# Optimization experiments

Hardware: AMD Instinct MI355X
Metric: run time of the kernel (lower is better)

Reference implementation:

```python
import jax, jax.numpy as jnp
import numpy as np

HIDDEN = 768
PDIM = int(HIDDEN / 4.67)  # 164
QK_DIM = 16
EPS = 1e-5


def setup_inputs() -> dict:
    key = jax.random.key(0)
    k_hs, k_qkv, k_out = jax.random.split(key, 3)
    B, S = 8, 2048
    hidden_states = jax.random.normal(k_hs, (B, S, HIDDEN), dtype=jnp.float32)
    qkv_out = 2 * QK_DIM + PDIM  # 196
    qkv_w = jax.random.normal(k_qkv, (qkv_out, PDIM), dtype=jnp.float32) * (PDIM ** -0.5)
    qkv_b = jnp.zeros((qkv_out,), dtype=jnp.float32)
    out_w = jax.random.normal(k_out, (HIDDEN, HIDDEN), dtype=jnp.float32) * (HIDDEN ** -0.5)
    out_b = jnp.zeros((HIDDEN,), dtype=jnp.float32)
    ln_scale = jnp.ones((PDIM,), dtype=jnp.float32)
    ln_bias = jnp.zeros((PDIM,), dtype=jnp.float32)
    return {
        "hidden_states": hidden_states,
        "ln_scale": ln_scale,
        "ln_bias": ln_bias,
        "qkv_w": qkv_w,
        "qkv_b": qkv_b,
        "out_w": out_w,
        "out_b": out_b,
    }


def reference(hidden_states, ln_scale, ln_bias, qkv_w, qkv_b, out_w, out_b):
    # channel split
    x1 = hidden_states[..., :PDIM]   # [B,S,pdim]
    x2 = hidden_states[..., PDIM:]   # [B,S,hidden-pdim]
    # LayerNorm over last dim
    mean = jnp.mean(x1, axis=-1, keepdims=True)
    var = jnp.mean(jnp.square(x1 - mean), axis=-1, keepdims=True)
    x1n = (x1 - mean) * jax.lax.rsqrt(var + EPS) * ln_scale + ln_bias
    # qkv projection: [B,S,2*qk+pdim]
    qkv = jnp.einsum("bsd,od->bso", x1n, qkv_w) + qkv_b
    q = qkv[..., :QK_DIM]
    k = qkv[..., QK_DIM:2 * QK_DIM]
    v = qkv[..., 2 * QK_DIM:]
    scale = QK_DIM ** -0.5
    scores = jnp.einsum("bqd,bkd->bqk", q, k) * scale  # [B,S,S]
    probs = jax.nn.softmax(scores, axis=-1)
    attended = jnp.einsum("bqk,bkd->bqd", probs, v)  # [B,S,pdim]
    merged = jnp.concatenate([attended, x2], axis=-1)  # [B,S,hidden]
    out = jnp.einsum("bsd,od->bso", merged, out_w) + out_b
    return out
```

## Files before the change

kernel.cpp:

```cpp
#include <hip/hip_runtime.h>
#include <hip/hip_bf16.h>

#define HID 768
#define PD 164
#define NQ 196
#define SEQ 2048

typedef __attribute__((ext_vector_type(8))) short bf16x8_t;
typedef __attribute__((ext_vector_type(4))) float f32x4_t;
typedef __attribute__((ext_vector_type(16))) float f32x16_t;
typedef __attribute__((ext_vector_type(4))) unsigned int u32x4_t;

static __device__ __forceinline__ unsigned short f2bfu(float f) {
  union { __hip_bfloat16 h; unsigned short u; } cv;
  cv.h = __float2bfloat16(f);
  return cv.u;
}

static __device__ __forceinline__ unsigned cvtpk(float a, float b) {
  unsigned r;
  asm("v_cvt_pk_bf16_f32 %0, %1, %2" : "=v"(r) : "v"(a), "v"(b));
  return r;
}

static __device__ __forceinline__ void gload16(const void* g, void* l) {
  __builtin_amdgcn_global_load_lds(
      (const __attribute__((address_space(1))) void*)g,
      (__attribute__((address_space(3))) void*)l, 16, 0, 0);
}

__global__ __launch_bounds__(256) void k_prep(const float* __restrict__ qkv_w,
                                              const float* __restrict__ out_w,
                                              unsigned short* __restrict__ qwb,
                                              unsigned short* __restrict__ wb) {
  int bid = blockIdx.x;
  if (bid < 576) {
    int i = (bid * 256 + threadIdx.x) * 4;
    float4 v = *(const float4*)(out_w + i);
    ushort4 o;
    o.x = f2bfu(v.x); o.y = f2bfu(v.y); o.z = f2bfu(v.z); o.w = f2bfu(v.w);
    *(ushort4*)(wb + i) = o;
  } else {
    int i = ((bid - 576) * 256 + threadIdx.x) * 4;
    int n = i / 192, k = i - n * 192;
    float v0 = (n < NQ && k + 0 < PD) ? qkv_w[n * PD + k + 0] : 0.f;
    float v1 = (n < NQ && k + 1 < PD) ? qkv_w[n * PD + k + 1] : 0.f;
    float v2 = (n < NQ && k + 2 < PD) ? qkv_w[n * PD + k + 2] : 0.f;
    float v3 = (n < NQ && k + 3 < PD) ? qkv_w[n * PD + k + 3] : 0.f;
    ushort4 o;
    o.x = f2bfu(v0); o.y = f2bfu(v1); o.z = f2bfu(v2); o.w = f2bfu(v3);
    *(ushort4*)(qwb + i) = o;
  }
}

__global__ __launch_bounds__(256) void k_ln(const float* __restrict__ hidden,
                                            const float* __restrict__ lns,
                                            const float* __restrict__ lnb,
                                            unsigned short* __restrict__ x1n,
                                            unsigned short* __restrict__ merged) {
  __shared__ float xr[64][172];
  __shared__ float stats[64][2];
  int t = threadIdx.x;
  int r0 = blockIdx.x * 64;
  #pragma unroll
  for (int i = 0; i < 11; i++) {
    int idx = t + i * 256;
    if (idx < 2624) {
      int row = idx / 41, q = idx - row * 41;
      float4 v = *(const float4*)(hidden + (size_t)(r0 + row) * HID + q * 4);
      *(float4*)&xr[row][q * 4] = v;
    }
  }
  __syncthreads();
  {
    int l = t & 63, w = t >> 6;
    int row = w * 16 + (l & 15), g = l >> 4;
    float sum = 0.f, sq = 0.f;
    #pragma unroll
    for (int j = 0; j < 41; j++) {
      float x = xr[row][g * 41 + j];
      sum += x; sq += x * x;
    }
    sum += __shfl_xor(sum, 16, 64); sum += __shfl_xor(sum, 32, 64);
    sq  += __shfl_xor(sq, 16, 64);  sq  += __shfl_xor(sq, 32, 64);
    float mean = sum * (1.f / PD);
    float var = sq * (1.f / PD) - mean * mean;
    float rstd = rsqrtf(var + 1e-5f);
    if (g == 0) { stats[row][0] = mean; stats[row][1] = rstd; }
  }
  __syncthreads();
  #pragma unroll
  for (int i = 0; i < 24; i++) {
    int idx = t + i * 256;
    int row = idx / 96, c2 = idx - row * 96;
    int d = c2 * 2;
    float mean = stats[row][0], rstd = stats[row][1];
    float v0 = (d < PD)     ? (xr[row][d]     - mean) * rstd * lns[d]     + lnb[d]     : 0.f;
    float v1 = (d + 1 < PD) ? (xr[row][d + 1] - mean) * rstd * lns[d + 1] + lnb[d + 1] : 0.f;
    unsigned int pk = (unsigned int)f2bfu(v0) | ((unsigned int)f2bfu(v1) << 16);
    *(unsigned int*)(x1n + (size_t)(r0 + row) * 192 + d) = pk;
  }
  #pragma unroll
  for (int i = 0; i < 38; i++) {
    int idx = t + i * 256;
    if (idx < 9664) {
      int row = idx / 151, q = idx - row * 151;
      int d = PD + q * 4;
      float4 v = *(const float4*)(hidden + (size_t)(r0 + row) * HID + d);
      ushort4 o;
      o.x = f2bfu(v.x); o.y = f2bfu(v.y); o.z = f2bfu(v.z); o.w = f2bfu(v.w);
      *(ushort4*)(merged + (size_t)(r0 + row) * HID + d) = o;
    }
  }
}

__global__ __launch_bounds__(256) void k_qkv(const unsigned short* __restrict__ x1n,
                                             const unsigned short* __restrict__ qwb,
                                             const float* __restrict__ qkv_b,
                                             unsigned short* __restrict__ qg,
                                             unsigned short* __restrict__ kg,
                                             unsigned short* __restrict__ v16) {
  __shared__ unsigned short Al[64 * 64];
  __shared__ unsigned short Bl[208 * 64];
  int t = threadIdx.x;
  int m0 = blockIdx.x * 64;
  int l = t & 63, w = t >> 6;
  f32x4_t acc[13];
  #pragma unroll
  for (int n = 0; n < 13; n++) acc[n] = (f32x4_t){0.f, 0.f, 0.f, 0.f};
  for (int ks = 0; ks < 3; ks++) {
    #pragma unroll
    for (int i = 0; i < 2; i++) {
      int off = t + i * 256;
      int row = off >> 3, c = off & 7;
      gload16(x1n + (size_t)(m0 + row) * 192 + ks * 64 + c * 8, (char*)Al + off * 16);
    }
    #pragma unroll
    for (int i = 0; i < 7; i++) {
      int off = t + i * 256;
      if (off < 1664) {
        int row = off >> 3, c = off & 7;
        gload16(qwb + (size_t)row * 192 + ks * 64 + c * 8, (char*)Bl + off * 16);
      }
    }
    __syncthreads();
    #pragma unroll
    for (int kc = 0; kc < 2; kc++) {
      bf16x8_t a = *(const bf16x8_t*)(Al + (w * 16 + (l & 15)) * 64 + kc * 32 + (l >> 4) * 8);
      #pragma unroll
      for (int n = 0; n < 13; n++) {
        bf16x8_t b = *(const bf16x8_t*)(Bl + (n * 16 + (l & 15)) * 64 + kc * 32 + (l >> 4) * 8);
        acc[n] = __builtin_amdgcn_mfma_f32_16x16x32_bf16(a, b, acc[n], 0, 0, 0);
      }
    }
    __syncthreads();
  }
  int g = l >> 4, lr15 = l & 15;
  {
    float bias = qkv_b[lr15];
    #pragma unroll
    for (int r = 0; r < 4; r++) {
      int grow = m0 + w * 16 + g * 4 + r;
      qg[(size_t)grow * 16 + lr15] = f2bfu((acc[0][r] + bias) * 0.36067376022224085f);
    }
  }
  {
    float bias = qkv_b[16 + lr15];
    #pragma unroll
    for (int r = 0; r < 4; r++) {
      int grow = m0 + w * 16 + g * 4 + r;
      kg[(size_t)grow * 16 + lr15] = f2bfu(acc[1][r] + bias);
    }
  }
  int s0 = (m0 & 2047) + w * 16;
  int bb = m0 >> 11;
  size_t vrowbase = (size_t)(bb * 128 + (s0 >> 4)) * 192;
  #pragma unroll
  for (int n = 2; n < 13; n++) {
    int col = n * 16 + lr15;
    int d = col - 32;
    float bias = (col < NQ) ? qkv_b[col] : 0.f;
    float v0 = acc[n][0] + bias, v1 = acc[n][1] + bias;
    float v2 = acc[n][2] + bias, v3 = acc[n][3] + bias;
    if (d == 164) { v0 = v1 = v2 = v3 = 1.f; }
    else if (d >= PD) { v0 = v1 = v2 = v3 = 0.f; }
    ushort4 o;
    o.x = f2bfu(v0); o.y = f2bfu(v1); o.z = f2bfu(v2); o.w = f2bfu(v3);
    *(ushort4*)(v16 + (vrowbase + d) * 16 + g * 4) = o;
  }
}

__global__ __launch_bounds__(256, 2) void k_attn(const unsigned short* __restrict__ qg,
                                                 const unsigned short* __restrict__ kg,
                                                 const unsigned short* __restrict__ v16,
                                                 unsigned short* __restrict__ merged) {
  __shared__ float red[2][64 * 98];
  int t = threadIdx.x;
  int w = t >> 6, l = t & 63;
  int b = blockIdx.x & 7, qt = blockIdx.x >> 3;
  int lo = l & 31, hi = l >> 5;
  int qbase = b * SEQ + qt * 32;
  bf16x8_t qf = *(const bf16x8_t*)(qg + (size_t)(qbase + lo) * 16 + hi * 8);
  const unsigned short* kb = kg + (size_t)b * SEQ * 16;
  const unsigned short* vbb = v16 + (size_t)b * 128 * 192 * 16;
  f32x16_t zro;
  #pragma unroll
  for (int r = 0; r < 16; r++) zro[r] = 0.f;
  f32x16_t acc[6];
  #pragma unroll
  for (int f = 0; f < 6; f++) acc[f] = zro;

  int it0 = w * 8;
  bf16x8_t kf0 = *(const bf16x8_t*)(kb + (size_t)(it0 * 64 + lo) * 16 + hi * 8);
  bf16x8_t kf1 = *(const bf16x8_t*)(kb + (size_t)(it0 * 64 + 32 + lo) * 16 + hi * 8);
  bf16x8_t va[6], vb_[6];
  {
    const unsigned short* vt0 = vbb + (size_t)(it0 * 4) * (192 * 16) + hi * 8;
    #pragma unroll
    for (int f = 0; f < 6; f++) va[f] = *(const bf16x8_t*)(vt0 + (f * 32 + lo) * 16);
  }
  for (int it = it0; it < it0 + 8; ++it) {
    bf16x8_t nk0 = *(const bf16x8_t*)(kb + (size_t)((it + 1) * 64 + lo) * 16 + hi * 8);
    bf16x8_t nk1 = *(const bf16x8_t*)(kb + (size_t)((it + 1) * 64 + 32 + lo) * 16 + hi * 8);
    f32x16_t sc0 = __builtin_amdgcn_mfma_f32_32x32x16_bf16(kf0, qf, zro, 0, 0, 0);
    f32x16_t sc1 = __builtin_amdgcn_mfma_f32_32x32x16_bf16(kf1, qf, zro, 0, 0, 0);
    bf16x8_t pa[4];
    #pragma unroll
    for (int jt = 0; jt < 2; ++jt) {
      f32x16_t sc = jt ? sc1 : sc0;
      unsigned u[8];
      #pragma unroll
      for (int k = 0; k < 8; ++k)
        u[k] = cvtpk(exp2f(sc[2 * k]), exp2f(sc[2 * k + 1]));
      asm volatile("v_permlane32_swap_b32 %0, %1" : "+v"(u[0]), "+v"(u[2]));
      asm volatile("v_permlane32_swap_b32 %0, %1" : "+v"(u[1]), "+v"(u[3]));
      asm volatile("v_permlane32_swap_b32 %0, %1" : "+v"(u[4]), "+v"(u[6]));
      asm volatile("v_permlane32_swap_b32 %0, %1" : "+v"(u[5]), "+v"(u[7]));
      union { u32x4_t u4; bf16x8_t h8; } c0, c1;
      c0.u4 = (u32x4_t){u[0], u[1], u[2], u[3]};
      c1.u4 = (u32x4_t){u[4], u[5], u[6], u[7]};
      pa[jt * 2 + 0] = c0.h8;
      pa[jt * 2 + 1] = c1.h8;
    }
#define PV_STEP(JS, VCUR, VNXT, NT, NJS)                                            \
    {                                                                               \
      const unsigned short* vtn = vbb + (size_t)((NT) * 4 + (NJS)) * (192 * 16) + hi * 8; \
      _Pragma("unroll")                                                             \
      for (int f = 0; f < 6; f++) VNXT[f] = *(const bf16x8_t*)(vtn + (f * 32 + lo) * 16); \
      _Pragma("unroll")                                                             \
      for (int f = 0; f < 6; f++)                                                   \
        acc[f] = __builtin_amdgcn_mfma_f32_32x32x16_bf16(pa[JS], VCUR[f], acc[f], 0, 0, 0); \
    }
    PV_STEP(0, va,  vb_, it, 1)
    PV_STEP(1, vb_, va,  it, 2)
    PV_STEP(2, va,  vb_, it, 3)
    PV_STEP(3, vb_, va,  it + 1, 0)
#undef PV_STEP
    kf0 = nk0; kf1 = nk1;
  }

  if (w >= 2) {
    float* dst = &red[w - 2][l * 98];
    #pragma unroll
    for (int f = 0; f < 6; f++)
      #pragma unroll
      for (int r = 0; r < 16; r += 2)
        *(float2*)(dst + f * 16 + r) = make_float2(acc[f][r], acc[f][r + 1]);
  }
  __syncthreads();
  if (w < 2) {
    const float* src = &red[w][l * 98];
    #pragma unroll
    for (int f = 0; f < 6; f++)
      #pragma unroll
      for (int r = 0; r < 16; r += 2) {
        float2 v = *(const float2*)(src + f * 16 + r);
        acc[f][r] += v.x; acc[f][r + 1] += v.y;
      }
  }
  __syncthreads();
  if (w == 1) {
    float* dst = &red[0][l * 98];
    #pragma unroll
    for (int f = 0; f < 6; f++)
      #pragma unroll
      for (int r = 0; r < 16; r += 2)
        *(float2*)(dst + f * 16 + r) = make_float2(acc[f][r], acc[f][r + 1]);
  }
  __syncthreads();
  if (w == 0) {
    const float* src = &red[0][l * 98];
    #pragma unroll
    for (int f = 0; f < 6; f++)
      #pragma unroll
      for (int r = 0; r < 16; r += 2) {
        float2 v = *(const float2*)(src + f * 16 + r);
        acc[f][r] += v.x; acc[f][r + 1] += v.y;
      }
    float dninv[16];
    #pragma unroll
    for (int r = 0; r < 16; ++r)
      dninv[r] = 1.0f / __shfl(acc[5][r], 4 + hi * 32, 64);
    #pragma unroll
    for (int f = 0; f < 6; ++f) {
      int d = f * 32 + lo;
      if (d < PD) {
        #pragma unroll
        for (int r = 0; r < 16; ++r) {
          int q = qbase + (r & 3) + 8 * (r >> 2) + 4 * hi;
          merged[(size_t)q * HID + d] = f2bfu(acc[f][r] * dninv[r]);
        }
      }
    }
  }
}

__global__ __launch_bounds__(256) void k_out(const unsigned short* __restrict__ mg,
                                             const unsigned short* __restrict__ wb,
                                             const float* __restrict__ out_b,
                                             float* __restrict__ out) {
  __shared__ unsigned short Al[2][128 * 64];
  __shared__ unsigned short Bl[2][128 * 64];
  int t = threadIdx.x;
  int bid = blockIdx.x;
  int wgid = (bid & 7) * 96 + (bid >> 3);
  int nb = wgid % 6, mb = wgid / 6;
  int m0 = mb * 128, n0 = nb * 128;
  int l = t & 63, w = t >> 6, wr = w >> 1, wc = w & 1;
  int lr = l & 15, lg = l >> 4;
  f32x4_t acc[4][4];
  #pragma unroll
  for (int mi = 0; mi < 4; mi++)
    #pragma unroll
    for (int ni = 0; ni < 4; ni++) acc[mi][ni] = (f32x4_t){0.f, 0.f, 0.f, 0.f};

  auto stage = [&](int buf, int kt) {
    #pragma unroll
    for (int i = 0; i < 4; i++) {
      int off = t + i * 256;
      int row = off >> 3, c = off & 7;
      int cs = c ^ (row & 7);
      gload16(mg + (size_t)(m0 + row) * HID + kt * 64 + cs * 8, (char*)&Al[buf][0] + off * 16);
    }
    #pragma unroll
    for (int i = 0; i < 4; i++) {
      int off = t + i * 256;
      int row = off >> 3, c = off & 7;
      int cs = c ^ (row & 7);
      gload16(wb + (size_t)(n0 + row) * HID + kt * 64 + cs * 8, (char*)&Bl[buf][0] + off * 16);
    }
  };
  auto compute = [&](int cur) {
    __builtin_amdgcn_s_setprio(1);
    #pragma unroll
    for (int kc = 0; kc < 2; kc++) {
      bf16x8_t a[4], bfr[4];
      #pragma unroll
      for (int mi = 0; mi < 4; mi++)
        a[mi] = *(const bf16x8_t*)(&Al[cur][(wr * 64 + mi * 16 + lr) * 64 + (((kc * 4 + lg) ^ (lr & 7)) * 8)]);
      #pragma unroll
      for (int ni = 0; ni < 4; ni++)
        bfr[ni] = *(const bf16x8_t*)(&Bl[cur][(wc * 64 + ni * 16 + lr) * 64 + (((kc * 4 + lg) ^ (lr & 7)) * 8)]);
      #pragma unroll
      for (int mi = 0; mi < 4; mi++)
        #pragma unroll
        for (int ni = 0; ni < 4; ni++)
          acc[mi][ni] = __builtin_amdgcn_mfma_f32_16x16x32_bf16(a[mi], bfr[ni], acc[mi][ni], 0, 0, 0);
    }
    __builtin_amdgcn_s_setprio(0);
  };

  stage(0, 0);
  stage(1, 1);
  for (int kt = 0; kt < 11; kt++) {
    int cur = kt & 1;
    asm volatile("s_waitcnt vmcnt(8)" ::: "memory");
    __builtin_amdgcn_sched_barrier(0);
    __builtin_amdgcn_s_barrier();
    compute(cur);
    asm volatile("s_waitcnt lgkmcnt(0)" ::: "memory");
    __builtin_amdgcn_sched_barrier(0);
    __builtin_amdgcn_s_barrier();
    if (kt + 2 < 12) stage(cur, kt + 2);
  }
  asm volatile("s_waitcnt vmcnt(0)" ::: "memory");
  __builtin_amdgcn_sched_barrier(0);
  __builtin_amdgcn_s_barrier();
  compute(1);

  #pragma unroll
  for (int ni = 0; ni < 4; ni++) {
    int col = n0 + wc * 64 + ni * 16 + lr;
    float bias = out_b[col];
    #pragma unroll
    for (int mi = 0; mi < 4; mi++) {
      #pragma unroll
      for (int r = 0; r < 4; r++) {
        int row = m0 + wr * 64 + mi * 16 + lg * 4 + r;
        out[(size_t)row * HID + col] = acc[mi][ni][r] + bias;
      }
    }
  }
}

extern "C" void kernel_launch(void* const* d_in, const int* in_sizes, int n_in,
                              void* d_out, int out_size, void* d_ws, size_t ws_size,
                              hipStream_t stream) {
  const float* hidden = (const float*)d_in[0];
  const float* lns    = (const float*)d_in[1];
  const float* lnb    = (const float*)d_in[2];
  const float* qkv_w  = (const float*)d_in[3];
  const float* qkv_b  = (const float*)d_in[4];
  const float* out_w  = (const float*)d_in[5];
  const float* out_b  = (const float*)d_in[6];
  char* ws = (char*)d_ws;
  unsigned short* qg  = (unsigned short*)(ws + 0);
  unsigned short* kg  = (unsigned short*)(ws + 524288);
  unsigned short* v16 = (unsigned short*)(ws + 1048576);
  unsigned short* x1n = (unsigned short*)(ws + 7340032);
  unsigned short* qwb = (unsigned short*)(ws + 13631488);
  unsigned short* wb  = (unsigned short*)(ws + 13711360);
  unsigned short* mg  = (unsigned short*)(ws + 14891008);
  hipLaunchKernelGGL(k_prep, dim3(615), dim3(256), 0, stream, qkv_w, out_w, qwb, wb);
  hipLaunchKernelGGL(k_ln,   dim3(256), dim3(256), 0, stream, hidden, lns, lnb, x1n, mg);
  hipLaunchKernelGGL(k_qkv,  dim3(256), dim3(256), 0, stream, x1n, qwb, qkv_b, qg, kg, v16);
  hipLaunchKernelGGL(k_attn, dim3(512), dim3(256), 0, stream, qg, kg, v16, mg);
  hipLaunchKernelGGL(k_out,  dim3(768), dim3(256), 0, stream, mg, wb, out_b, (float*)d_out);
}
```

Baseline: 100.6 us.

## Fuse LayerNorm and QKV projection into one kernel via shared memory

Merges the LayerNorm kernel and the QKV GEMM kernel so the normalized bf16 activations stay in LDS instead of round-tripping through a global x1n buffer. The weight operand is now read directly from global memory per MFMA rather than staged through LDS, and one kernel launch is removed. This saves a global write and read of the normalized activations plus a launch gap. The cost is higher LDS use per block and uncoalesced, repeated global weight loads, which mostly hit cache.

```diff
diff --git a/kernel.cpp b/kernel.cpp
--- a/kernel.cpp
+++ b/kernel.cpp
@@ -53,13 +53,18 @@
   }
 }
 
-__global__ __launch_bounds__(256) void k_ln(const float* __restrict__ hidden,
-                                            const float* __restrict__ lns,
-                                            const float* __restrict__ lnb,
-                                            unsigned short* __restrict__ x1n,
-                                            unsigned short* __restrict__ merged) {
+__global__ __launch_bounds__(256, 2) void k_lnqkv(const float* __restrict__ hidden,
+                                                  const float* __restrict__ lns,
+                                                  const float* __restrict__ lnb,
+                                                  const unsigned short* __restrict__ qwb,
+                                                  const float* __restrict__ qkv_b,
+                                                  unsigned short* __restrict__ merged,
+                                                  unsigned short* __restrict__ qg,
+                                                  unsigned short* __restrict__ kg,
+                                                  unsigned short* __restrict__ v16) {
   __shared__ float xr[64][172];
   __shared__ float stats[64][2];
+  __shared__ unsigned short Aq[64][200];
   int t = threadIdx.x;
   int r0 = blockIdx.x * 64;
   #pragma unroll
@@ -98,7 +103,7 @@
     float v0 = (d < PD)     ? (xr[row][d]     - mean) * rstd * lns[d]     + lnb[d]     : 0.f;
     float v1 = (d + 1 < PD) ? (xr[row][d + 1] - mean) * rstd * lns[d + 1] + lnb[d + 1] : 0.f;
     unsigned int pk = (unsigned int)f2bfu(v0) | ((unsigned int)f2bfu(v1) << 16);
-    *(unsigned int*)(x1n + (size_t)(r0 + row) * 192 + d) = pk;
+    *(unsigned int*)(&Aq[row][d]) = pk;
   }
   #pragma unroll
   for (int i = 0; i < 38; i++) {
@@ -112,55 +117,25 @@
       *(ushort4*)(merged + (size_t)(r0 + row) * HID + d) = o;
     }
   }
-}
-
-__global__ __launch_bounds__(256) void k_qkv(const unsigned short* __restrict__ x1n,
-                                             const unsigned short* __restrict__ qwb,
-                                             const float* __restrict__ qkv_b,
-                                             unsigned short* __restrict__ qg,
-                                             unsigned short* __restrict__ kg,
-                                             unsigned short* __restrict__ v16) {
-  __shared__ unsigned short Al[64 * 64];
-  __shared__ unsigned short Bl[208 * 64];
-  int t = threadIdx.x;
-  int m0 = blockIdx.x * 64;
-  int l = t & 63, w = t >> 6;
+  __syncthreads();
+  int l = t & 63, w = t >> 6, lr15 = l & 15, g = l >> 4;
   f32x4_t acc[13];
   #pragma unroll
   for (int n = 0; n < 13; n++) acc[n] = (f32x4_t){0.f, 0.f, 0.f, 0.f};
-  for (int ks = 0; ks < 3; ks++) {
-    #pragma unroll
-    for (int i = 0; i < 2; i++) {
-      int off = t + i * 256;
-      int row = off >> 3, c = off & 7;
-      gload16(x1n + (size_t)(m0 + row) * 192 + ks * 64 + c * 8, (char*)Al + off * 16);
-    }
-    #pragma unroll
-    for (int i = 0; i < 7; i++) {
-      int off = t + i * 256;
-      if (off < 1664) {
-        int row = off >> 3, c = off & 7;
-        gload16(qwb + (size_t)row * 192 + ks * 64 + c * 8, (char*)Bl + off * 16);
-      }
-    }
-    __syncthreads();
-    #pragma unroll
-    for (int kc = 0; kc < 2; kc++) {
-      bf16x8_t a = *(const bf16x8_t*)(Al + (w * 16 + (l & 15)) * 64 + kc * 32 + (l >> 4) * 8);
-      #pragma unroll
-      for (int n = 0; n < 13; n++) {
-        bf16x8_t b = *(const bf16x8_t*)(Bl + (n * 16 + (l & 15)) * 64 + kc * 32 + (l >> 4) * 8);
-        acc[n] = __builtin_amdgcn_mfma_f32_16x16x32_bf16(a, b, acc[n], 0, 0, 0);
-      }
-    }
-    __syncthreads();
-  }
-  int g = l >> 4, lr15 = l & 15;
+  #pragma unroll 2
+  for (int kc = 0; kc < 6; kc++) {
+    bf16x8_t a = *(const bf16x8_t*)(&Aq[w * 16 + lr15][kc * 32 + g * 8]);
+    #pragma unroll
+    for (int n = 0; n < 13; n++) {
+      bf16x8_t b = *(const bf16x8_t*)(qwb + (size_t)(n * 16 + lr15) * 192 + kc * 32 + g * 8);
+      acc[n] = __builtin_amdgcn_mfma_f32_16x16x32_bf16(a, b, acc[n], 0, 0, 0);
+    }
+  }
   {
     float bias = qkv_b[lr15];
     #pragma unroll
     for (int r = 0; r < 4; r++) {
-      int grow = m0 + w * 16 + g * 4 + r;
+      int grow = r0 + w * 16 + g * 4 + r;
       qg[(size_t)grow * 16 + lr15] = f2bfu((acc[0][r] + bias) * 0.36067376022224085f);
     }
   }
@@ -168,12 +143,12 @@
     float bias = qkv_b[16 + lr15];
     #pragma unroll
     for (int r = 0; r < 4; r++) {
-      int grow = m0 + w * 16 + g * 4 + r;
+      int grow = r0 + w * 16 + g * 4 + r;
       kg[(size_t)grow * 16 + lr15] = f2bfu(acc[1][r] + bias);
     }
   }
-  int s0 = (m0 & 2047) + w * 16;
-  int bb = m0 >> 11;
+  int s0 = (r0 & 2047) + w * 16;
+  int bb = r0 >> 11;
   size_t vrowbase = (size_t)(bb * 128 + (s0 >> 4)) * 192;
   #pragma unroll
   for (int n = 2; n < 13; n++) {
@@ -417,13 +392,12 @@
   unsigned short* qg  = (unsigned short*)(ws + 0);
   unsigned short* kg  = (unsigned short*)(ws + 524288);
   unsigned short* v16 = (unsigned short*)(ws + 1048576);
-  unsigned short* x1n = (unsigned short*)(ws + 7340032);
   unsigned short* qwb = (unsigned short*)(ws + 13631488);
   unsigned short* wb  = (unsigned short*)(ws + 13711360);
   unsigned short* mg  = (unsigned short*)(ws + 14891008);
-  hipLaunchKernelGGL(k_prep, dim3(615), dim3(256), 0, stream, qkv_w, out_w, qwb, wb);
-  hipLaunchKernelGGL(k_ln,   dim3(256), dim3(256), 0, stream, hidden, lns, lnb, x1n, mg);
-  hipLaunchKernelGGL(k_qkv,  dim3(256), dim3(256), 0, stream, x1n, qwb, qkv_b, qg, kg, v16);
-  hipLaunchKernelGGL(k_attn, dim3(512), dim3(256), 0, stream, qg, kg, v16, mg);
-  hipLaunchKernelGGL(k_out,  dim3(768), dim3(256), 0, stream, mg, wb, out_b, (float*)d_out);
-}
+  hipLaunchKernelGGL(k_prep,  dim3(615), dim3(256), 0, stream, qkv_w, out_w, qwb, wb);
+  hipLaunchKernelGGL(k_lnqkv, dim3(256), dim3(256), 0, stream, hidden, lns, lnb, qwb, qkv_b,
+                     mg, qg, kg, v16);
+  hipLaunchKernelGGL(k_attn,  dim3(512), dim3(256), 0, stream, qg, kg, v16, mg);
+  hipLaunchKernelGGL(k_out,   dim3(768), dim3(256), 0, stream, mg, wb, out_b, (float*)d_out);
+}
```

New measurement: 99.55 us. No clear change (-1.0%).
